# Performance work log

Hardware: AMD Instinct MI355X
Metric: run time of the kernel (lower is better)

## Reference

```python
import jax, jax.numpy as jnp
import numpy as np

NUM_GROUPS = 32
EPS = 1e-6


def group_norm(x, gamma, beta):
    # x: [B, C, H, W]; GroupNorm over (channels-in-group, H, W)
    B, C, H, W = x.shape
    xg = x.reshape(B, NUM_GROUPS, C // NUM_GROUPS, H, W)
    mean = xg.mean(axis=(2, 3, 4), keepdims=True)
    var = xg.var(axis=(2, 3, 4), keepdims=True)
    xn = ((xg - mean) * jax.lax.rsqrt(var + EPS)).reshape(B, C, H, W)
    return xn * gamma[None, :, None, None] + beta[None, :, None, None]


def conv1x1(x, w, b):
    # 1x1 conv == channel-mixing matmul. w: [C_out, C_in]
    return jnp.einsum('bchw,oc->bohw', x, w) + b[None, :, None, None]


def setup_inputs() -> dict:
    key = jax.random.key(0)
    ks = jax.random.split(key, 6)
    B, C, H, W = 8, 256, 64, 64
    s = 1.0 / np.sqrt(C)  # fan-in scaled weights (like Conv2d default)
    inp = {
        'x': jax.random.normal(ks[0], (B, C, H, W), jnp.float32),
        'gamma': jnp.ones((C,), jnp.float32),
        'beta': jnp.zeros((C,), jnp.float32),
        'wq': jax.random.normal(ks[1], (C, C), jnp.float32) * s,
        'bq': jnp.zeros((C,), jnp.float32),
        'wk': jax.random.normal(ks[2], (C, C), jnp.float32) * s,
        'bk': jnp.zeros((C,), jnp.float32),
        'wv': jax.random.normal(ks[3], (C, C), jnp.float32) * s,
        'bv': jnp.zeros((C,), jnp.float32),
        'wo': jax.random.normal(ks[4], (C, C), jnp.float32) * s,
        'bo': jnp.zeros((C,), jnp.float32),
    }
    return inp


def reference(x, gamma, beta, wq, bq, wk, bk, wv, bv, wo, bo):
    B, C, H, W = x.shape
    h = group_norm(x, gamma, beta)
    q = conv1x1(h, wq, bq)
    k = conv1x1(h, wk, bk)
    v = conv1x1(h, wv, bv)
    # elu + 1 feature map (nonnegative kernel features)
    q = jax.nn.elu(q) + 1.0
    k = jax.nn.elu(k) + 1.0
    N = H * W
    kf = k.reshape(B, C, N)            # [B, C, N]
    vf = v.reshape(B, C, N)            # [B, C, N]
    qf = q.reshape(B, C, N)            # [B, C, N]
    # kv = k @ v^T : [B, C, C]
    kv = jnp.einsum('bcn,bdn->bcd', kf, vf)
    # h_out[b, n, d] = sum_c q[b, c, n] * kv[b, c, d]; stored channel-first
    h_out = jnp.einsum('bcn,bcd->bdn', qf, kv).reshape(B, C, H, W)
    return x + conv1x1(h_out, wo, bo)
```

## Files before the change

kernel.cpp:

```cpp
#include <hip/hip_runtime.h>
#include <math.h>

#define C_DIM 256
#define N_DIM 4096
#define B_DIM 8

typedef __attribute__((ext_vector_type(8))) short bf16x8;
typedef __attribute__((ext_vector_type(4))) float f32x4;
typedef __attribute__((ext_vector_type(8))) unsigned short us8;
typedef __attribute__((ext_vector_type(4))) unsigned short us4;

__device__ inline unsigned short f2bf(float f) {
    unsigned int u = __float_as_uint(f);
    u += 0x7fffu + ((u >> 16) & 1u);
    return (unsigned short)(u >> 16);
}

__device__ inline void gload_lds16(const void* g, void* l) {
    __builtin_amdgcn_global_load_lds(
        (const __attribute__((address_space(1))) unsigned int*)g,
        (__attribute__((address_space(3))) unsigned int*)l, 16, 0, 0);
}

__global__ __launch_bounds__(256) void transx(const float* __restrict__ x,
                                              unsigned short* __restrict__ xT,
                                              float2* __restrict__ pst) {
    int b = blockIdx.y, nt = blockIdx.x, n0 = nt * 64;
    int t = threadIdx.x;
    __shared__ unsigned short trans[64][264];

    #pragma unroll
    for (int it = 0; it < 16; it++) {
        int c  = it*16 + (t >> 4);
        int nl = (t & 15) * 4;
        float4 v = *(const float4*)(x + ((size_t)(b*C_DIM + c))*N_DIM + n0 + nl);
        trans[nl+0][c] = f2bf(v.x);
        trans[nl+1][c] = f2bf(v.y);
        trans[nl+2][c] = f2bf(v.z);
        trans[nl+3][c] = f2bf(v.w);
        float s4 = v.x + v.y + v.z + v.w;
        float q4 = v.x*v.x + v.y*v.y + v.z*v.z + v.w*v.w;
        #pragma unroll
        for (int m = 1; m < 16; m <<= 1) {
            s4 += __shfl_xor(s4, m);
            q4 += __shfl_xor(q4, m);
        }
        if ((t & 15) == 0)
            pst[(size_t)(b*64 + nt)*256 + c] = make_float2(s4, q4);
    }
    __syncthreads();

    #pragma unroll
    for (int it = 0; it < 8; it++) {
        int nl = it*8 + (t >> 5);
        int cb = (t & 31) * 8;
        us8 vv = *(us8*)&trans[nl][cb];
        *(us8*)(xT + ((size_t)b*N_DIM + n0 + nl)*C_DIM + cb) = vv;
    }
}

__global__ __launch_bounds__(256) void fold(
    const float* __restrict__ wq, const float* __restrict__ wk,
    const float* __restrict__ wv, const float* __restrict__ wo,
    const float* __restrict__ bq, const float* __restrict__ bk,
    const float* __restrict__ bv,
    const float* __restrict__ gamma, const float* __restrict__ beta,
    const float2* __restrict__ pst,
    unsigned short* __restrict__ wqb2, unsigned short* __restrict__ wkvb2,
    unsigned short* __restrict__ wob,
    float* __restrict__ bq2, float* __restrict__ bkv2)
{
    int z = blockIdx.y;
    int t = threadIdx.x;
    if (z == 12) {
        int base = blockIdx.x * 8192;
        #pragma unroll
        for (int i = 0; i < 8; i++) {
            int idx = base + i*1024 + t*4;
            float4 v = *(const float4*)(wo + idx);
            us4 r; r[0]=f2bf(v.x); r[1]=f2bf(v.y); r[2]=f2bf(v.z); r[3]=f2bf(v.w);
            *(us4*)(wob + idx) = r;
        }
        return;
    }
    int b = blockIdx.x;
    __shared__ float scale[256], shift[256], chS[256], chQ[256];

    float S = 0.f, Q = 0.f;
    for (int nt = 0; nt < 64; nt++) {
        float2 u = pst[(size_t)(b*64 + nt)*256 + t];
        S += u.x; Q += u.y;
    }
    chS[t] = S; chQ[t] = Q;
    __syncthreads();
    {
        int gb = t & ~7;
        float Sg = 0.f, Qg = 0.f;
        #pragma unroll
        for (int j = 0; j < 8; j++) { Sg += chS[gb+j]; Qg += chQ[gb+j]; }
        float mean = Sg * (1.f/32768.f);
        float var  = Qg * (1.f/32768.f) - mean*mean;
        float inv  = rsqrtf(var + 1e-6f);
        float sc = gamma[t] * inv;
        scale[t] = sc;
        shift[t] = beta[t] - mean * sc;
    }
    __syncthreads();

    int r0 = z * 64;
    const float* Wsrc; const float* bsrc; unsigned short* dst; float* bdst;
    if (r0 < 256)      { int r=r0;     Wsrc=wq+(size_t)r*256; bsrc=bq+r; dst=wqb2 +(size_t)b*65536 +(size_t)r*256;      bdst=bq2 +b*256+r; }
    else if (r0 < 512) { int r=r0-256; Wsrc=wk+(size_t)r*256; bsrc=bk+r; dst=wkvb2+(size_t)b*131072+(size_t)r*256;      bdst=bkv2+b*512+r; }
    else               { int r=r0-512; Wsrc=wv+(size_t)r*256; bsrc=bv+r; dst=wkvb2+(size_t)b*131072+(size_t)(r+256)*256; bdst=bkv2+b*512+256+r; }

    #pragma unroll
    for (int i = 0; i < 16; i++) {
        int idx = t + 256*i;
        int row = idx >> 6, c4 = (idx & 63) * 4;
        float4 v = *(const float4*)(Wsrc + (size_t)row*256 + c4);
        us4 r;
        r[0] = f2bf(v.x * scale[c4+0]);
        r[1] = f2bf(v.y * scale[c4+1]);
        r[2] = f2bf(v.z * scale[c4+2]);
        r[3] = f2bf(v.w * scale[c4+3]);
        *(us4*)(dst + (size_t)row*256 + c4) = r;
    }

    {
        int row = t >> 2, qd = t & 3;
        float p = 0.f;
        for (int i = 0; i < 64; i++) {
            int c = qd*64 + i;
            p += Wsrc[(size_t)row*256 + c] * shift[c];
        }
        chS[t] = p;
        __syncthreads();
        if (t < 64)
            bdst[t] = bsrc[t] + chS[t*4] + chS[t*4+1] + chS[t*4+2] + chS[t*4+3];
    }
}

__global__ __launch_bounds__(256) void kvred(const float* __restrict__ src, unsigned short* __restrict__ dst) {
    int gi = (blockIdx.x * 256 + threadIdx.x) * 4;
    int b = gi >> 16, idx = gi & 65535;
    float4 a = make_float4(0.f,0.f,0.f,0.f);
    #pragma unroll
    for (int sp = 0; sp < 16; sp++) {
        float4 v = *(const float4*)(src + (((size_t)b*16 + sp) << 16) + idx);
        a.x += v.x; a.y += v.y; a.z += v.z; a.w += v.w;
    }
    us4 r; r[0] = f2bf(a.x); r[1] = f2bf(a.y); r[2] = f2bf(a.z); r[3] = f2bf(a.w);
    *(us4*)(dst + ((size_t)b << 16) + idx) = r;
}

template<int MODE>
__device__ __forceinline__ void gemm_body(
    const unsigned short* __restrict__ Ab, const unsigned short* __restrict__ Bb,
    const float* __restrict__ bias, const float* __restrict__ residb,
    void* __restrict__ Cb,
    int N, int K, int k0, int Ks, int m_blk, int n_blk, bool elu,
    char* smem)
{
    unsigned short* As0 = (unsigned short*)smem;
    unsigned short* Bs0 = As0 + 4096;
    unsigned short* As1 = As0 + 8192;
    unsigned short* Bs1 = As0 + 12288;

    int t = threadIdx.x;
    int w = t >> 6, l = t & 63;
    int wm = w >> 1, wn = w & 1;
    int l15 = l & 15, quad = l >> 4;

    int srow = w * 16 + (l >> 2);
    int skc  = (l & 3) * 8;

    f32x4 acc[4][4];
    #pragma unroll
    for (int i = 0; i < 4; i++)
        #pragma unroll
        for (int j = 0; j < 4; j++)
            #pragma unroll
            for (int r = 0; r < 4; r++) acc[i][j][r] = 0.f;

    int fro = (wm*64 + l15)*32 + quad*8;
    int fco = (wn*64 + l15)*32 + quad*8;
    int sl  = w*512 + l*8;

    for (int kt = k0; kt < k0 + Ks; kt += 64) {
        #pragma unroll
        for (int rep = 0; rep < 2; rep++) {
            size_t ga = (size_t)(m_blk + rep*64 + srow) * K + kt + skc;
            size_t gb = (size_t)(n_blk + rep*64 + srow) * K + kt + skc;
            gload_lds16(Ab + ga,      As0 + sl + rep*2048);
            gload_lds16(Bb + gb,      Bs0 + sl + rep*2048);
            gload_lds16(Ab + ga + 32, As1 + sl + rep*2048);
            gload_lds16(Bb + gb + 32, Bs1 + sl + rep*2048);
        }
        __syncthreads();
        {
            bf16x8 af[4], bfr[4];
            #pragma unroll
            for (int i = 0; i < 4; i++) af[i]  = *(const bf16x8*)(As0 + fro + i*512);
            #pragma unroll
            for (int j = 0; j < 4; j++) bfr[j] = *(const bf16x8*)(Bs0 + fco + j*512);
            #pragma unroll
            for (int i = 0; i < 4; i++)
                #pragma unroll
                for (int j = 0; j < 4; j++)
                    acc[i][j] = __builtin_amdgcn_mfma_f32_16x16x32_bf16(af[i], bfr[j], acc[i][j], 0, 0, 0);
            #pragma unroll
            for (int i = 0; i < 4; i++) af[i]  = *(const bf16x8*)(As1 + fro + i*512);
            #pragma unroll
            for (int j = 0; j < 4; j++) bfr[j] = *(const bf16x8*)(Bs1 + fco + j*512);
            #pragma unroll
            for (int i = 0; i < 4; i++)
                #pragma unroll
                for (int j = 0; j < 4; j++)
                    acc[i][j] = __builtin_amdgcn_mfma_f32_16x16x32_bf16(af[i], bfr[j], acc[i][j], 0, 0, 0);
        }
        __syncthreads();
    }

    if (MODE == 0 || MODE == 1 || MODE == 4) {
        unsigned short* ep = (unsigned short*)smem;
        int row0 = wm*64 + quad*4;
        int col0 = wn*64 + l15;
        #pragma unroll
        for (int i = 0; i < 4; i++) {
            #pragma unroll
            for (int j = 0; j < 4; j++) {
                int cl = col0 + j*16;
                #pragma unroll
                for (int r = 0; r < 4; r++) {
                    int rl = row0 + i*16 + r;
                    float val = acc[i][j][r];
                    if (MODE == 0) {
                        val += bias[n_blk + cl];
                        val = val > 0.f ? val + 1.f : __expf(val);
                    } else if (MODE == 1) {
                        val += bias[m_blk + rl];
                        if (elu) val = val > 0.f ? val + 1.f : __expf(val);
                    }
                    ep[rl*136 + cl] = f2bf(val);
                }
            }
        }
        __syncthreads();
        unsigned short* Cp = (unsigned short*)Cb;
        #pragma unroll
        for (int it = 0; it < 8; it++) {
            int row = it*16 + (t >> 4);
            int col = (t & 15) * 8;
            us8 vv = *(us8*)(ep + row*136 + col);
            *(us8*)(Cp + (size_t)(m_blk + row) * N + n_blk + col) = vv;
        }
    } else {
        float* ep32 = (float*)smem;
        float* Cp = (float*)Cb;
        #pragma unroll
        for (int h = 0; h < 2; h++) {
            if (wm == h) {
                int row0 = quad*4;
                int col0 = wn*64 + l15;
                #pragma unroll
                for (int i = 0; i < 4; i++)
                    #pragma unroll
                    for (int j = 0; j < 4; j++)
                        #pragma unroll
                        for (int r = 0; r < 4; r++)
                            ep32[(row0 + i*16 + r)*140 + col0 + j*16] = acc[i][j][r];
            }
            __syncthreads();
            #pragma unroll
            for (int it = 0; it < 8; it++) {
                int rl  = it*8 + (t >> 5);
                int row = m_blk + h*64 + rl;
                int col = (t & 31) * 4;
                f32x4 vv = *(f32x4*)(ep32 + rl*140 + col);
                if (MODE == 5) {
                    float bi = bias[row];
                    float4 rv = *(const float4*)(residb + (size_t)row * N + n_blk + col);
                    vv[0] += bi + rv.x; vv[1] += bi + rv.y;
                    vv[2] += bi + rv.z; vv[3] += bi + rv.w;
                }
                *(f32x4*)(Cp + (size_t)row * N + n_blk + col) = vv;
            }
            __syncthreads();
        }
    }
}

__global__ __launch_bounds__(256) void qkv_kernel(
    const unsigned short* __restrict__ xT,
    const unsigned short* __restrict__ wqb2, const unsigned short* __restrict__ wkvb2,
    const float* __restrict__ bq2, const float* __restrict__ bkv2,
    unsigned short* __restrict__ qT, unsigned short* __restrict__ kvbuf)
{
    __shared__ __align__(16) char smem[36864];
    int z = blockIdx.x;
    if (z < 512) {
        int b = z >> 6, rem = z & 63;
        int m_blk = (rem >> 1) * 128, n_blk = (rem & 1) * 128;
        gemm_body<0>(xT + (size_t)b*1048576, wqb2 + (size_t)b*65536,
                     bq2 + b*256, nullptr,
                     qT + (size_t)b*1048576,
                     256, 256, 0, 256, m_blk, n_blk, true, smem);
    } else {
        int iz = z - 512;
        int b = iz >> 7, rem = iz & 127;
        int m_blk = (rem >> 5) * 128, n_blk = (rem & 31) * 128;
        gemm_body<1>(wkvb2 + (size_t)b*131072, xT + (size_t)b*1048576,
                     bkv2 + b*512, nullptr,
                     kvbuf + (size_t)b*2097152,
                     4096, 256, 0, 256, m_blk, n_blk, m_blk < 256, smem);
    }
}

__global__ __launch_bounds__(256) void kv_kernel(const unsigned short* __restrict__ kvbuf,
                                                 float* __restrict__ kvf)
{
    __shared__ __align__(16) char smem[36864];
    int b = blockIdx.z >> 4, sp = blockIdx.z & 15;
    gemm_body<3>(kvbuf + (size_t)b*2097152, kvbuf + (size_t)b*2097152 + 1048576,
                 nullptr, nullptr,
                 kvf + (size_t)(b*16 + sp)*65536,
                 256, 4096, sp*256, 256, blockIdx.y*128, blockIdx.x*128, false, smem);
}

__global__ __launch_bounds__(256) void m2_kernel(const unsigned short* __restrict__ wob,
                                                 const unsigned short* __restrict__ kvb,
                                                 unsigned short* __restrict__ M2b)
{
    __shared__ __align__(16) char smem[36864];
    int b = blockIdx.z;
    gemm_body<4>(wob, kvb + (size_t)b*65536,
                 nullptr, nullptr,
                 M2b + (size_t)b*65536,
                 256, 256, 0, 256, blockIdx.y*128, blockIdx.x*128, false, smem);
}

__global__ __launch_bounds__(256) void out_kernel(const unsigned short* __restrict__ M2b,
                                                  const unsigned short* __restrict__ qT,
                                                  const float* __restrict__ bo,
                                                  const float* __restrict__ x,
                                                  float* __restrict__ outp)
{
    __shared__ __align__(16) char smem[36864];
    int b = blockIdx.z;
    gemm_body<5>(M2b + (size_t)b*65536, qT + (size_t)b*1048576,
                 bo, x + (size_t)b*1048576,
                 outp + (size_t)b*1048576,
                 4096, 256, 0, 256, blockIdx.y*128, blockIdx.x*128, false, smem);
}

extern "C" void kernel_launch(void* const* d_in, const int* in_sizes, int n_in,
                              void* d_out, int out_size, void* d_ws, size_t ws_size,
                              hipStream_t stream) {
    const float* x     = (const float*)d_in[0];
    const float* gamma = (const float*)d_in[1];
    const float* beta  = (const float*)d_in[2];
    const float* wq    = (const float*)d_in[3];
    const float* bq    = (const float*)d_in[4];
    const float* wk    = (const float*)d_in[5];
    const float* bk    = (const float*)d_in[6];
    const float* wv    = (const float*)d_in[7];
    const float* bv    = (const float*)d_in[8];
    const float* wo    = (const float*)d_in[9];
    const float* bo    = (const float*)d_in[10];
    float* out = (float*)d_out;

    const size_t TEN = (size_t)B_DIM * C_DIM * N_DIM;
    unsigned short* ws16  = (unsigned short*)d_ws;
    unsigned short* xT    = ws16;
    unsigned short* qT    = xT    + TEN;
    unsigned short* kvbuf = qT    + TEN;
    unsigned short* wqb2  = kvbuf + 2*TEN;
    unsigned short* wkvb2 = wqb2  + 524288;
    unsigned short* wob   = wkvb2 + 1048576;
    unsigned short* M2b   = wob   + 65536;
    unsigned short* kvb   = M2b   + 524288;
    float*          bq2   = (float*)(kvb + 524288);
    float*          bkv2  = bq2   + 2048;
    float2*         pst   = (float2*)(bkv2 + 4096);
    float*          kvf   = (float*)(pst + 131072);

    transx<<<dim3(64, B_DIM), 256, 0, stream>>>(x, xT, pst);
    fold<<<dim3(8, 13), 256, 0, stream>>>(wq, wk, wv, wo, bq, bk, bv, gamma, beta,
                                          pst, wqb2, wkvb2, wob, bq2, bkv2);
    qkv_kernel<<<dim3(1536), 256, 0, stream>>>(xT, wqb2, wkvb2, bq2, bkv2, qT, kvbuf);
    kv_kernel<<<dim3(2, 2, B_DIM*16), 256, 0, stream>>>(kvbuf, kvf);
    kvred<<<dim3(512), 256, 0, stream>>>(kvf, kvb);
    m2_kernel<<<dim3(2, 2, B_DIM), 256, 0, stream>>>(wob, kvb, M2b);
    out_kernel<<<dim3(32, 2, B_DIM), 256, 0, stream>>>(M2b, qT, bo, x, out);
}
```

Measured before the change: 187.7 us.

## Double-buffer GEMM LDS tiles to overlap global loads with MFMA

The GEMM main loop now uses a software pipeline over two LDS buffers, each a 32-wide K slice. While the current buffer feeds the MFMAs, the next slice is fetched into the other buffer with direct global-to-LDS loads. Before, each 64-wide K step loaded both halves, synchronized, computed, then synchronized again, so loads and compute never overlapped. The trade-off is less compute per iteration to hide each load behind. Correctness depends on the barrier waiting for the async LDS loads to finish.

```diff
diff --git a/kernel.cpp b/kernel.cpp
--- a/kernel.cpp
+++ b/kernel.cpp
@@ -161,10 +161,10 @@
     int N, int K, int k0, int Ks, int m_blk, int n_blk, bool elu,
     char* smem)
 {
-    unsigned short* As0 = (unsigned short*)smem;
-    unsigned short* Bs0 = As0 + 4096;
-    unsigned short* As1 = As0 + 8192;
-    unsigned short* Bs1 = As0 + 12288;
+    unsigned short* SA0 = (unsigned short*)smem;
+    unsigned short* SB0 = SA0 + 4096;
+    unsigned short* SA1 = SA0 + 8192;
+    unsigned short* SB1 = SA0 + 12288;
 
     int t = threadIdx.x;
     int w = t >> 6, l = t & 63;
@@ -186,40 +186,41 @@
     int fco = (wn*64 + l15)*32 + quad*8;
     int sl  = w*512 + l*8;
 
-    for (int kt = k0; kt < k0 + Ks; kt += 64) {
-        #pragma unroll
-        for (int rep = 0; rep < 2; rep++) {
-            size_t ga = (size_t)(m_blk + rep*64 + srow) * K + kt + skc;
-            size_t gb = (size_t)(n_blk + rep*64 + srow) * K + kt + skc;
-            gload_lds16(Ab + ga,      As0 + sl + rep*2048);
-            gload_lds16(Bb + gb,      Bs0 + sl + rep*2048);
-            gload_lds16(Ab + ga + 32, As1 + sl + rep*2048);
-            gload_lds16(Bb + gb + 32, Bs1 + sl + rep*2048);
-        }
+    const unsigned short* Abase = Ab + (size_t)(m_blk + srow) * K + skc + k0;
+    const unsigned short* Bbase = Bb + (size_t)(n_blk + srow) * K + skc + k0;
+    const size_t rstep = (size_t)64 * K;
+
+    gload_lds16(Abase,         SA0 + sl);
+    gload_lds16(Abase + rstep, SA0 + sl + 2048);
+    gload_lds16(Bbase,         SB0 + sl);
+    gload_lds16(Bbase + rstep, SB0 + sl + 2048);
+
+    int nIter = Ks >> 5;
+    for (int it = 0; it < nIter; it++) {
         __syncthreads();
-        {
-            bf16x8 af[4], bfr[4];
+        const unsigned short* Ac = (it & 1) ? SA1 : SA0;
+        const unsigned short* Bc = (it & 1) ? SB1 : SB0;
+        if (it + 1 < nIter) {
+            int kn = (it + 1) * 32;
+            unsigned short* An = (it & 1) ? SA0 : SA1;
+            unsigned short* Bn = (it & 1) ? SB0 : SB1;
+            gload_lds16(Abase + kn,         An + sl);
+            gload_lds16(Abase + rstep + kn, An + sl + 2048);
+            gload_lds16(Bbase + kn,         Bn + sl);
+            gload_lds16(Bbase + rstep + kn, Bn + sl + 2048);
+        }
+        bf16x8 af[4], bfr[4];
+        #pragma unroll
+        for (int i = 0; i < 4; i++) af[i]  = *(const bf16x8*)(Ac + fro + i*512);
+        #pragma unroll
+        for (int j = 0; j < 4; j++) bfr[j] = *(const bf16x8*)(Bc + fco + j*512);
+        #pragma unroll
+        for (int i = 0; i < 4; i++)
             #pragma unroll
-            for (int i = 0; i < 4; i++) af[i]  = *(const bf16x8*)(As0 + fro + i*512);
-            #pragma unroll
-            for (int j = 0; j < 4; j++) bfr[j] = *(const bf16x8*)(Bs0 + fco + j*512);
-            #pragma unroll
-            for (int i = 0; i < 4; i++)
-                #pragma unroll
-                for (int j = 0; j < 4; j++)
-                    acc[i][j] = __builtin_amdgcn_mfma_f32_16x16x32_bf16(af[i], bfr[j], acc[i][j], 0, 0, 0);
-            #pragma unroll
-            for (int i = 0; i < 4; i++) af[i]  = *(const bf16x8*)(As1 + fro + i*512);
-            #pragma unroll
-            for (int j = 0; j < 4; j++) bfr[j] = *(const bf16x8*)(Bs1 + fco + j*512);
-            #pragma unroll
-            for (int i = 0; i < 4; i++)
-                #pragma unroll
-                for (int j = 0; j < 4; j++)
-                    acc[i][j] = __builtin_amdgcn_mfma_f32_16x16x32_bf16(af[i], bfr[j], acc[i][j], 0, 0, 0);
-        }
-        __syncthreads();
-    }
+            for (int j = 0; j < 4; j++)
+                acc[i][j] = __builtin_amdgcn_mfma_f32_16x16x32_bf16(af[i], bfr[j], acc[i][j], 0, 0, 0);
+    }
+    __syncthreads();
 
     if (MODE == 0 || MODE == 1 || MODE == 4) {
         unsigned short* ep = (unsigned short*)smem;
```

After: 190.4 us. About the same (+1.4%).

## Avoid materializing V by computing K·x then folding Wv into kv

Applied to the files above, without the earlier changes.

V is no longer materialized. The pipeline computes K·x^T over the spatial dimension (x stored as a channel-first bf16 copy), then multiplies by the folded Wv and adds the bias term through a per-row K sum, which is accumulated with atomics in the K epilogue. This removes the V projection GEMM and its writes from the large QKV stage and adds one small 256x256 GEMM per batch. The residual in the output epilogue now reads the bf16 copy of x instead of fp32 x, which cuts read bandwidth but lowers the precision of the residual add.

```diff
diff --git a/kernel.cpp b/kernel.cpp
--- a/kernel.cpp
+++ b/kernel.cpp
@@ -15,6 +15,9 @@
     u += 0x7fffu + ((u >> 16) & 1u);
     return (unsigned short)(u >> 16);
 }
+__device__ inline float bf2f(unsigned short u) {
+    return __uint_as_float(((unsigned int)u) << 16);
+}
 
 __device__ inline void gload_lds16(const void* g, void* l) {
     __builtin_amdgcn_global_load_lds(
@@ -24,6 +27,7 @@
 
 __global__ __launch_bounds__(256) void transx(const float* __restrict__ x,
                                               unsigned short* __restrict__ xT,
+                                              unsigned short* __restrict__ xbf,
                                               float2* __restrict__ pst) {
     int b = blockIdx.y, nt = blockIdx.x, n0 = nt * 64;
     int t = threadIdx.x;
@@ -34,10 +38,11 @@
         int c  = it*16 + (t >> 4);
         int nl = (t & 15) * 4;
         float4 v = *(const float4*)(x + ((size_t)(b*C_DIM + c))*N_DIM + n0 + nl);
-        trans[nl+0][c] = f2bf(v.x);
-        trans[nl+1][c] = f2bf(v.y);
-        trans[nl+2][c] = f2bf(v.z);
-        trans[nl+3][c] = f2bf(v.w);
+        unsigned short b0 = f2bf(v.x), b1 = f2bf(v.y), b2 = f2bf(v.z), b3 = f2bf(v.w);
+        trans[nl+0][c] = b0; trans[nl+1][c] = b1;
+        trans[nl+2][c] = b2; trans[nl+3][c] = b3;
+        us4 r4; r4[0]=b0; r4[1]=b1; r4[2]=b2; r4[3]=b3;
+        *(us4*)(xbf + ((size_t)(b*C_DIM + c))*N_DIM + n0 + nl) = r4;
         float s4 = v.x + v.y + v.z + v.w;
         float q4 = v.x*v.x + v.y*v.y + v.z*v.z + v.w*v.w;
         #pragma unroll
@@ -68,7 +73,7 @@
     const float2* __restrict__ pst,
     unsigned short* __restrict__ wqb2, unsigned short* __restrict__ wkvb2,
     unsigned short* __restrict__ wob,
-    float* __restrict__ bq2, float* __restrict__ bkv2)
+    float* __restrict__ bq2, float* __restrict__ bkv2, float* __restrict__ ksum)
 {
     int z = blockIdx.y;
     int t = threadIdx.x;
@@ -81,6 +86,7 @@
             us4 r; r[0]=f2bf(v.x); r[1]=f2bf(v.y); r[2]=f2bf(v.z); r[3]=f2bf(v.w);
             *(us4*)(wob + idx) = r;
         }
+        ksum[blockIdx.x*256 + t] = 0.f;
         return;
     }
     int b = blockIdx.x;
@@ -140,7 +146,7 @@
     }
 }
 
-__global__ __launch_bounds__(256) void kvred(const float* __restrict__ src, unsigned short* __restrict__ dst) {
+__global__ __launch_bounds__(256) void kxred(const float* __restrict__ src, unsigned short* __restrict__ dst) {
     int gi = (blockIdx.x * 256 + threadIdx.x) * 4;
     int b = gi >> 16, idx = gi & 65535;
     float4 a = make_float4(0.f,0.f,0.f,0.f);
@@ -156,9 +162,9 @@
 template<int MODE>
 __device__ __forceinline__ void gemm_body(
     const unsigned short* __restrict__ Ab, const unsigned short* __restrict__ Bb,
-    const float* __restrict__ bias, const float* __restrict__ residb,
+    const float* __restrict__ bias, void* __restrict__ aux,
     void* __restrict__ Cb,
-    int N, int K, int k0, int Ks, int m_blk, int n_blk, bool elu,
+    int N, int K, int k0, int Ks, int m_blk, int n_blk,
     char* smem)
 {
     unsigned short* As0 = (unsigned short*)smem;
@@ -221,12 +227,13 @@
         __syncthreads();
     }
 
-    if (MODE == 0 || MODE == 1 || MODE == 4) {
+    if (MODE == 0 || MODE == 2 || MODE == 4 || MODE == 6) {
         unsigned short* ep = (unsigned short*)smem;
         int row0 = wm*64 + quad*4;
         int col0 = wn*64 + l15;
         #pragma unroll
         for (int i = 0; i < 4; i++) {
+            float rsum[4] = {0.f, 0.f, 0.f, 0.f};
             #pragma unroll
             for (int j = 0; j < 4; j++) {
                 int cl = col0 + j*16;
@@ -237,11 +244,26 @@
                     if (MODE == 0) {
                         val += bias[n_blk + cl];
                         val = val > 0.f ? val + 1.f : __expf(val);
-                    } else if (MODE == 1) {
+                    } else if (MODE == 2) {
                         val += bias[m_blk + rl];
-                        if (elu) val = val > 0.f ? val + 1.f : __expf(val);
+                        val = val > 0.f ? val + 1.f : __expf(val);
+                        rsum[r] += val;
+                    } else if (MODE == 6) {
+                        val += bias[m_blk + rl] * ((const float*)aux)[n_blk + cl];
                     }
                     ep[rl*136 + cl] = f2bf(val);
+                }
+            }
+            if (MODE == 2) {
+                #pragma unroll
+                for (int r = 0; r < 4; r++) {
+                    float s = rsum[r];
+                    s += __shfl_xor(s, 1);
+                    s += __shfl_xor(s, 2);
+                    s += __shfl_xor(s, 4);
+                    s += __shfl_xor(s, 8);
+                    if (l15 == 0)
+                        atomicAdd((float*)aux + m_blk + row0 + i*16 + r, s);
                 }
             }
         }
@@ -277,11 +299,11 @@
                 int row = m_blk + h*64 + rl;
                 int col = (t & 31) * 4;
                 f32x4 vv = *(f32x4*)(ep32 + rl*140 + col);
-                if (MODE == 5) {
+                if (MODE == 7) {
                     float bi = bias[row];
-                    float4 rv = *(const float4*)(residb + (size_t)row * N + n_blk + col);
-                    vv[0] += bi + rv.x; vv[1] += bi + rv.y;
-                    vv[2] += bi + rv.z; vv[3] += bi + rv.w;
+                    us4 rv = *(const us4*)((const unsigned short*)aux + (size_t)row * N + n_blk + col);
+                    vv[0] += bi + bf2f(rv[0]); vv[1] += bi + bf2f(rv[1]);
+                    vv[2] += bi + bf2f(rv[2]); vv[3] += bi + bf2f(rv[3]);
                 }
                 *(f32x4*)(Cp + (size_t)row * N + n_blk + col) = vv;
             }
@@ -290,11 +312,12 @@
     }
 }
 
-__global__ __launch_bounds__(256) void qkv_kernel(
+__global__ __launch_bounds__(256) void qk_kernel(
     const unsigned short* __restrict__ xT,
     const unsigned short* __restrict__ wqb2, const unsigned short* __restrict__ wkvb2,
     const float* __restrict__ bq2, const float* __restrict__ bkv2,
-    unsigned short* __restrict__ qT, unsigned short* __restrict__ kvbuf)
+    unsigned short* __restrict__ qT, unsigned short* __restrict__ kb,
+    float* __restrict__ ksum)
 {
     __shared__ __align__(16) char smem[36864];
     int z = blockIdx.x;
@@ -304,27 +327,42 @@
         gemm_body<0>(xT + (size_t)b*1048576, wqb2 + (size_t)b*65536,
                      bq2 + b*256, nullptr,
                      qT + (size_t)b*1048576,
-                     256, 256, 0, 256, m_blk, n_blk, true, smem);
+                     256, 256, 0, 256, m_blk, n_blk, smem);
     } else {
         int iz = z - 512;
-        int b = iz >> 7, rem = iz & 127;
+        int b = iz >> 6, rem = iz & 63;
         int m_blk = (rem >> 5) * 128, n_blk = (rem & 31) * 128;
-        gemm_body<1>(wkvb2 + (size_t)b*131072, xT + (size_t)b*1048576,
-                     bkv2 + b*512, nullptr,
-                     kvbuf + (size_t)b*2097152,
-                     4096, 256, 0, 256, m_blk, n_blk, m_blk < 256, smem);
-    }
-}
-
-__global__ __launch_bounds__(256) void kv_kernel(const unsigned short* __restrict__ kvbuf,
-                                                 float* __restrict__ kvf)
+        gemm_body<2>(wkvb2 + (size_t)b*131072, xT + (size_t)b*1048576,
+                     bkv2 + b*512, ksum + b*256,
+                     kb + (size_t)b*1048576,
+                     4096, 256, 0, 256, m_blk, n_blk, smem);
+    }
+}
+
+__global__ __launch_bounds__(256) void kx_kernel(const unsigned short* __restrict__ kb,
+                                                 const unsigned short* __restrict__ xbf,
+                                                 float* __restrict__ kxf)
 {
     __shared__ __align__(16) char smem[36864];
     int b = blockIdx.z >> 4, sp = blockIdx.z & 15;
-    gemm_body<3>(kvbuf + (size_t)b*2097152, kvbuf + (size_t)b*2097152 + 1048576,
+    gemm_body<3>(kb + (size_t)b*1048576, xbf + (size_t)b*1048576,
                  nullptr, nullptr,
-                 kvf + (size_t)(b*16 + sp)*65536,
-                 256, 4096, sp*256, 256, blockIdx.y*128, blockIdx.x*128, false, smem);
+                 kxf + (size_t)(b*16 + sp)*65536,
+                 256, 4096, sp*256, 256, blockIdx.y*128, blockIdx.x*128, smem);
+}
+
+__global__ __launch_bounds__(256) void kv_kernel(const unsigned short* __restrict__ kxb,
+                                                 const unsigned short* __restrict__ wkvb2,
+                                                 const float* __restrict__ ksum,
+                                                 const float* __restrict__ bkv2,
+                                                 unsigned short* __restrict__ kvb)
+{
+    __shared__ __align__(16) char smem[36864];
+    int b = blockIdx.z;
+    gemm_body<6>(kxb + (size_t)b*65536, wkvb2 + (size_t)b*131072 + 65536,
+                 ksum + b*256, (void*)(bkv2 + b*512 + 256),
+                 kvb + (size_t)b*65536,
+                 256, 256, 0, 256, blockIdx.y*128, blockIdx.x*128, smem);
 }
 
 __global__ __launch_bounds__(256) void m2_kernel(const unsigned short* __restrict__ wob,
@@ -336,21 +374,21 @@
     gemm_body<4>(wob, kvb + (size_t)b*65536,
                  nullptr, nullptr,
                  M2b + (size_t)b*65536,
-                 256, 256, 0, 256, blockIdx.y*128, blockIdx.x*128, false, smem);
+                 256, 256, 0, 256, blockIdx.y*128, blockIdx.x*128, smem);
 }
 
 __global__ __launch_bounds__(256) void out_kernel(const unsigned short* __restrict__ M2b,
                                                   const unsigned short* __restrict__ qT,
                                                   const float* __restrict__ bo,
-                                                  const float* __restrict__ x,
+                                                  const unsigned short* __restrict__ xbf,
                                                   float* __restrict__ outp)
 {
     __shared__ __align__(16) char smem[36864];
     int b = blockIdx.z;
-    gemm_body<5>(M2b + (size_t)b*65536, qT + (size_t)b*1048576,
-                 bo, x + (size_t)b*1048576,
+    gemm_body<7>(M2b + (size_t)b*65536, qT + (size_t)b*1048576,
+                 bo, (void*)(xbf + (size_t)b*1048576),
                  outp + (size_t)b*1048576,
-                 4096, 256, 0, 256, blockIdx.y*128, blockIdx.x*128, false, smem);
+                 4096, 256, 0, 256, blockIdx.y*128, blockIdx.x*128, smem);
 }
 
 extern "C" void kernel_launch(void* const* d_in, const int* in_sizes, int n_in,
@@ -372,24 +410,28 @@
     const size_t TEN = (size_t)B_DIM * C_DIM * N_DIM;
     unsigned short* ws16  = (unsigned short*)d_ws;
     unsigned short* xT    = ws16;
-    unsigned short* qT    = xT    + TEN;
-    unsigned short* kvbuf = qT    + TEN;
-    unsigned short* wqb2  = kvbuf + 2*TEN;
+    unsigned short* xbf   = xT    + TEN;
+    unsigned short* qT    = xbf   + TEN;
+    unsigned short* kb    = qT    + TEN;
+    unsigned short* wqb2  = kb    + TEN;
     unsigned short* wkvb2 = wqb2  + 524288;
     unsigned short* wob   = wkvb2 + 1048576;
-    unsigned short* M2b   = wob   + 65536;
-    unsigned short* kvb   = M2b   + 524288;
-    float*          bq2   = (float*)(kvb + 524288);
+    unsigned short* kxb   = wob   + 65536;
+    unsigned short* kvb   = kxb   + 524288;
+    unsigned short* M2b   = kvb   + 524288;
+    float*          bq2   = (float*)(M2b + 524288);
     float*          bkv2  = bq2   + 2048;
-    float2*         pst   = (float2*)(bkv2 + 4096);
-    float*          kvf   = (float*)(pst + 131072);
-
-    transx<<<dim3(64, B_DIM), 256, 0, stream>>>(x, xT, pst);
+    float*          ksum  = bkv2  + 4096;
+    float2*         pst   = (float2*)(ksum + 2048);
+    float*          kxf   = (float*)(pst + 131072);
+
+    transx<<<dim3(64, B_DIM), 256, 0, stream>>>(x, xT, xbf, pst);
     fold<<<dim3(8, 13), 256, 0, stream>>>(wq, wk, wv, wo, bq, bk, bv, gamma, beta,
-                                          pst, wqb2, wkvb2, wob, bq2, bkv2);
-    qkv_kernel<<<dim3(1536), 256, 0, stream>>>(xT, wqb2, wkvb2, bq2, bkv2, qT, kvbuf);
-    kv_kernel<<<dim3(2, 2, B_DIM*16), 256, 0, stream>>>(kvbuf, kvf);
-    kvred<<<dim3(512), 256, 0, stream>>>(kvf, kvb);
+                                          pst, wqb2, wkvb2, wob, bq2, bkv2, ksum);
+    qk_kernel<<<dim3(1024), 256, 0, stream>>>(xT, wqb2, wkvb2, bq2, bkv2, qT, kb, ksum);
+    kx_kernel<<<dim3(2, 2, B_DIM*16), 256, 0, stream>>>(kb, xbf, kxf);
+    kxred<<<dim3(512), 256, 0, stream>>>(kxf, kxb);
+    kv_kernel<<<dim3(2, 2, B_DIM), 256, 0, stream>>>(kxb, wkvb2, ksum, bkv2, kvb);
     m2_kernel<<<dim3(2, 2, B_DIM), 256, 0, stream>>>(wob, kvb, M2b);
-    out_kernel<<<dim3(32, 2, B_DIM), 256, 0, stream>>>(M2b, qT, bo, x, out);
-}
+    out_kernel<<<dim3(32, 2, B_DIM), 256, 0, stream>>>(M2b, qT, bo, xbf, out);
+}
```

Result: slower. 194.0 us (+3.4%).
